# Kernel optimization log

Hardware: AMD Instinct MI355X
Metric: run time of the kernel (lower is better)

## Reference

```python
import jax, jax.numpy as jnp
import numpy as np

B, T_ENC, T_DEC = 64, 512, 400
IN_DIM, R = 80, 2
D_ENC, D_ATT, D_PRE = 256, 256, 128
NEG_INF = -1e9


def _gru(x, h, Wi, Wh, bi, bh):
    # PyTorch GRUCell math
    gi = x @ Wi + bi
    gh = h @ Wh + bh
    ir, iz, inn = jnp.split(gi, 3, axis=-1)
    hr, hz, hn = jnp.split(gh, 3, axis=-1)
    r = jax.nn.sigmoid(ir + hr)
    z = jax.nn.sigmoid(iz + hz)
    n = jnp.tanh(inn + r * hn)
    return (1.0 - z) * n + z * h


def setup_inputs() -> dict:
    key = jax.random.key(0)
    ks = jax.random.split(key, 32)
    s = 0.05
    d_in = IN_DIM * R
    inp = {
        "encoder_outputs": jax.random.normal(ks[0], (B, T_ENC, D_ENC), jnp.float32),
        "inputs": jax.random.normal(ks[1], (B, T_DEC, d_in), jnp.float32),
        "memory_lengths": jax.random.randint(ks[2], (B,), T_ENC // 2, T_ENC + 1).astype(jnp.int32),
        # prenet
        "pre_W1": s * jax.random.normal(ks[3], (d_in, 256), jnp.float32),
        "pre_b1": jnp.zeros((256,), jnp.float32),
        "pre_W2": s * jax.random.normal(ks[4], (256, 128), jnp.float32),
        "pre_b2": jnp.zeros((128,), jnp.float32),
        # Bahdanau attention
        "mem_W": s * jax.random.normal(ks[5], (D_ENC, D_ATT), jnp.float32),
        "q_W": s * jax.random.normal(ks[6], (256, D_ATT), jnp.float32),
        "v_W": s * jax.random.normal(ks[7], (D_ATT, 1), jnp.float32),
        # attention GRUCell: input = cat(prenet 128, attention 256) = 384
        "att_Wi": s * jax.random.normal(ks[8], (384, 768), jnp.float32),
        "att_Wh": s * jax.random.normal(ks[9], (256, 768), jnp.float32),
        "att_bi": jnp.zeros((768,), jnp.float32),
        "att_bh": jnp.zeros((768,), jnp.float32),
        # project_to_decoder_in
        "proj_in_W": s * jax.random.normal(ks[10], (512, 256), jnp.float32),
        "proj_in_b": jnp.zeros((256,), jnp.float32),
        # decoder GRUCells
        "dec1_Wi": s * jax.random.normal(ks[11], (256, 768), jnp.float32),
        "dec1_Wh": s * jax.random.normal(ks[12], (256, 768), jnp.float32),
        "dec1_bi": jnp.zeros((768,), jnp.float32),
        "dec1_bh": jnp.zeros((768,), jnp.float32),
        "dec2_Wi": s * jax.random.normal(ks[13], (256, 768), jnp.float32),
        "dec2_Wh": s * jax.random.normal(ks[14], (256, 768), jnp.float32),
        "dec2_bi": jnp.zeros((768,), jnp.float32),
        "dec2_bh": jnp.zeros((768,), jnp.float32),
        # output projections
        "mel_W": s * jax.random.normal(ks[15], (256, d_in), jnp.float32),
        "mel_b": jnp.zeros((d_in,), jnp.float32),
        "gate_W": s * jax.random.normal(ks[16], (256, R), jnp.float32),
        "gate_b": jnp.zeros((R,), jnp.float32),
    }
    return inp


def _decoder_forward(encoder_outputs, inputs, memory_lengths,
                     pre_W1, pre_b1, pre_W2, pre_b2,
                     mem_W, q_W, v_W,
                     att_Wi, att_Wh, att_bi, att_bh,
                     proj_in_W, proj_in_b,
                     dec1_Wi, dec1_Wh, dec1_bi, dec1_bh,
                     dec2_Wi, dec2_Wh, dec2_bi, dec2_bh,
                     mel_W, mel_b, gate_W, gate_b):
    Bq, Tq, _ = encoder_outputs.shape
    processed_memory = encoder_outputs @ mem_W  # (B, T_enc, D_att)
    valid = jnp.arange(Tq)[None, :] < memory_lengths[:, None]  # (B, T_enc)

    # teacher forcing: input at step t is inputs[t-1], zeros at t=0
    prev = jnp.concatenate([jnp.zeros_like(inputs[:, :1]), inputs[:, :-1]], axis=1)
    prev = jnp.swapaxes(prev, 0, 1)  # (T_dec, B, in_dim*r)

    def prenet(x):
        # dropout is identity in eval mode
        h = jax.nn.relu(x @ pre_W1 + pre_b1)
        return jax.nn.relu(h @ pre_W2 + pre_b2)

    def step(carry, x_prev):
        att_h, h1, h2, cur_att = carry
        pre = prenet(x_prev)  # (B, 128)
        cell_in = jnp.concatenate([pre, cur_att], axis=-1)  # (B, 384)
        att_h = _gru(cell_in, att_h, att_Wi, att_Wh, att_bi, att_bh)  # (B, 256)
        # Bahdanau alignment over encoder memory
        score = jnp.squeeze(
            jnp.tanh(processed_memory + (att_h @ q_W)[:, None, :]) @ v_W, -1)  # (B, T_enc)
        score = jnp.where(valid, score, NEG_INF)
        align = jax.nn.softmax(score, axis=-1)
        cur_att = jnp.einsum('bt,btd->bd', align, encoder_outputs)  # (B, 256)
        dec_in = jnp.concatenate([att_h, cur_att], axis=-1) @ proj_in_W + proj_in_b
        h1 = _gru(dec_in, h1, dec1_Wi, dec1_Wh, dec1_bi, dec1_bh)
        d = h1 + dec_in
        h2 = _gru(d, h2, dec2_Wi, dec2_Wh, dec2_bi, dec2_bh)
        d = h2 + d
        gate = jax.nn.sigmoid(d @ gate_W + gate_b)  # (B, r)
        out = d @ mel_W + mel_b  # (B, in_dim*r)
        return (att_h, h1, h2, cur_att), (out, align, gate)

    z = jnp.zeros((Bq, 256), encoder_outputs.dtype)
    init = (z, z, z, z)
    _, (outs, aligns, gates) = jax.lax.scan(step, init, prev)
    outputs = jnp.swapaxes(outs, 0, 1)      # (B, T_dec, in_dim*r)
    alignments = jnp.swapaxes(aligns, 0, 1)  # (B, T_dec, T_enc)
    gates = jnp.swapaxes(gates, 0, 1)        # (B, T_dec, r)
    return outputs, alignments, gates


def reference(encoder_outputs, inputs, memory_lengths,
              pre_W1, pre_b1, pre_W2, pre_b2,
              mem_W, q_W, v_W,
              att_Wi, att_Wh, att_bi, att_bh,
              proj_in_W, proj_in_b,
              dec1_Wi, dec1_Wh, dec1_bi, dec1_bh,
              dec2_Wi, dec2_Wh, dec2_bi, dec2_bh,
              mel_W, mel_b, gate_W, gate_b):
    return _decoder_forward(encoder_outputs, inputs, memory_lengths,
                            pre_W1, pre_b1, pre_W2, pre_b2,
                            mem_W, q_W, v_W,
                            att_Wi, att_Wh, att_bi, att_bh,
                            proj_in_W, proj_in_b,
                            dec1_Wi, dec1_Wh, dec1_bi, dec1_bh,
                            dec2_Wi, dec2_Wh, dec2_bi, dec2_bh,
                            mel_W, mel_b, gate_W, gate_b)
```

## Files before the change

kernel.cpp:

```cpp
#include <hip/hip_runtime.h>

#define TDEC 400
#define NTH 512
#define NWG 256

typedef float f32x4 __attribute__((ext_vector_type(4)));
typedef unsigned u32x4 __attribute__((ext_vector_type(4)));
typedef unsigned u32x2 __attribute__((ext_vector_type(2)));

#define OFF_BAR   0
#define OFF_ATTH  11264
#define OFF_H1    44032
#define OFF_H2    76800
#define OFF_CURP  109568
#define OFF_ATTS  125952
#define OFF_Q     126208
#define ZERO_FLOATS 142592
#define OFF_D1    142592
#define OFF_SUMS  158976
#define OFF_C1    184576
#define OFF_PRE   185600
#define OFF_PMB   1824000
#define OFF_ENCB  6018304
#define OFF_D2A   10212608
#define T_WIT_A   10212608
#define T_WHT_A   10507520
#define T_M1T     10704128
#define T_WHT1    11097344
#define T_PJT     11293952
#define T_WIT2    11425024
#define T_WHT2    11621632
#define T_QWT     11818240
#define T_M1      11883776
#define OFF_BLOB  16766208

#define BLOB_N   26112
#define BLOB_STR 26624
#define BO_AI  0
#define BO_AH  4608
#define BO_Q   7680
#define BO_M1  8704
#define BO_H1  14848
#define BO_PJ  17920
#define BO_I2  19968
#define BO_H2  23040

#define AOFF 4096000
#define GOFF 17203200

#define MSTI  (8*1024)
#define GENI  (9*1024)
#define FAILI (10*1024)

__device__ __forceinline__ float fsig(float x){ return 1.0f/(1.0f+__expf(-x)); }
__device__ __forceinline__ float ftanh(float x){ float e = __expf(2.0f*x); return 1.0f - 2.0f/(e+1.0f); }
__device__ __forceinline__ float blo(unsigned u){ return __uint_as_float(u<<16); }
__device__ __forceinline__ float bhi(unsigned u){ return __uint_as_float(u & 0xffff0000u); }

__device__ __forceinline__ f32x4 cload16(const float* p){
  f32x4 r;
  asm volatile("global_load_dwordx4 %0, %1, off sc0 sc1" : "=v"(r) : "v"(p));
  return r;
}
__device__ __forceinline__ f32x4 cload16w(const float* p){
  f32x4 r;
  asm volatile("global_load_dwordx4 %0, %1, off sc0 sc1\n\ts_waitcnt vmcnt(0)" : "=v"(r) : "v"(p));
  return r;
}
__device__ __forceinline__ u32x4 cload16u(const unsigned short* p){
  u32x4 r;
  asm volatile("global_load_dwordx4 %0, %1, off sc0 sc1" : "=v"(r) : "v"(p));
  return r;
}
__device__ __forceinline__ float aload4(const float* p){
  unsigned u = __hip_atomic_load((const unsigned*)p, __ATOMIC_RELAXED, __HIP_MEMORY_SCOPE_AGENT);
  return __uint_as_float(u);
}
__device__ __forceinline__ void astore4(float* p, float v){
  __hip_atomic_store((unsigned*)p, __float_as_uint(v), __ATOMIC_RELAXED, __HIP_MEMORY_SCOPE_AGENT);
}
__device__ __forceinline__ void aadd(float* p, float v){
  __hip_atomic_fetch_add(p, v, __ATOMIC_RELAXED, __HIP_MEMORY_SCOPE_AGENT);
}
__device__ __forceinline__ int aloadi(const int* p){
  return __hip_atomic_load(p, __ATOMIC_RELAXED, __HIP_MEMORY_SCOPE_AGENT);
}

__device__ __forceinline__ void ldsbar(){
  __builtin_amdgcn_sched_barrier(0);
  asm volatile("s_waitcnt lgkmcnt(0)" ::: "memory");
  __builtin_amdgcn_s_barrier();
  __builtin_amdgcn_sched_barrier(0);
}

__device__ __forceinline__ void gbar(int* bar, int wg, int n){
  asm volatile("s_waitcnt vmcnt(0)" ::: "memory");
  __syncthreads();
  if (threadIdx.x == 0){
    if (aloadi(&bar[FAILI]) == 0){
      int a = __hip_atomic_fetch_add(&bar[(wg&7)*1024], 1, __ATOMIC_RELAXED, __HIP_MEMORY_SCOPE_AGENT);
      if (a == 32*n - 1){
        int m = __hip_atomic_fetch_add(&bar[MSTI], 1, __ATOMIC_RELAXED, __HIP_MEMORY_SCOPE_AGENT);
        if (m == 8*n - 1)
          __hip_atomic_store(&bar[GENI], n, __ATOMIC_RELAXED, __HIP_MEMORY_SCOPE_AGENT);
      }
      int sp = 0;
      while (aloadi(&bar[GENI]) < n){
        __builtin_amdgcn_s_sleep(1);
        if (++sp > (1<<20)){
          __hip_atomic_store(&bar[FAILI], 1, __ATOMIC_RELAXED, __HIP_MEMORY_SCOPE_AGENT);
          break;
        }
      }
    }
  }
  __syncthreads();
}

__device__ __forceinline__ unsigned short f2bf(float f){
  unsigned u = __float_as_uint(f);
  return (unsigned short)((u + 0x7fffu + ((u>>16)&1u)) >> 16);
}

template<int N8>
__device__ __forceinline__ float bdot(const unsigned short* wr, const float* xr){
  f32x4 accA = 0.f, accB = 0.f;
  #pragma unroll 4
  for (int k = 0; k < N8; ++k){
    u32x4 u = *(const u32x4*)(wr + k*8);
    f32x4 a = *(const f32x4*)(xr + k*8);
    f32x4 b = *(const f32x4*)(xr + k*8 + 4);
    f32x4 w0, w1;
    w0[0]=blo(u[0]); w0[1]=bhi(u[0]); w0[2]=blo(u[1]); w0[3]=bhi(u[1]);
    w1[0]=blo(u[2]); w1[1]=bhi(u[2]); w1[2]=blo(u[3]); w1[3]=bhi(u[3]);
    accA += w0*a; accB += w1*b;
  }
  f32x4 s = accA + accB;
  return s[0]+s[1]+s[2]+s[3];
}

__global__ __launch_bounds__(256, 1) void transpose_k(const float* __restrict__ in,
                                                      float* __restrict__ outp, int K, int C){
  __shared__ float tl[32][33];
  int c0 = blockIdx.x * 32, k0 = blockIdx.y * 32;
  int tx = threadIdx.x & 31, ty = threadIdx.x >> 5;
  for (int i = ty; i < 32; i += 8){
    int k = k0 + i, c = c0 + tx;
    if (k < K && c < C) tl[i][tx] = in[k * C + c];
  }
  __syncthreads();
  for (int i = ty; i < 32; i += 8){
    int c = c0 + i, k = k0 + tx;
    if (c < C && k < K) outp[c * K + k] = tl[tx][i];
  }
}

__global__ __launch_bounds__(128, 1) void fuse_k(const float* __restrict__ projW,
    const float* __restrict__ d1Wi, float* __restrict__ M1){
  int jt = blockIdx.x % 6, i = blockIdx.x / 6;
  int j = jt * 128 + threadIdx.x;
  float acc = 0.f;
  for (int k = 0; k < 256; ++k) acc += projW[i*256+k] * d1Wi[k*768+j];
  M1[i*768+j] = acc;
}

__global__ __launch_bounds__(256, 1) void c1_k(const float* __restrict__ projB,
    const float* __restrict__ d1Wi, const float* __restrict__ d1Bi, float* __restrict__ C1){
  int j = blockIdx.x * 256 + threadIdx.x;
  float acc = d1Bi[j];
  for (int k = 0; k < 256; ++k) acc += projB[k] * d1Wi[k*768+j];
  C1[j] = acc;
}

__global__ __launch_bounds__(512, 1) void pack_k(float* __restrict__ ws){
  int sl = blockIdx.x;
  const float* TAI = ws + T_WIT_A;
  const float* TAH = ws + T_WHT_A;
  const float* TM1 = ws + T_M1T;
  const float* TH1 = ws + T_WHT1;
  const float* TPJ = ws + T_PJT;
  const float* TI2 = ws + T_WIT2;
  const float* TH2 = ws + T_WHT2;
  const float* TQ  = ws + T_QWT;
  unsigned short* blob = (unsigned short*)(ws + OFF_BLOB) + (size_t)sl * BLOB_STR;
  for (int idx = threadIdx.x; idx < BLOB_N; idx += 512){
    float v; int cs, k, o;
    if (idx < BO_AH){ cs = idx / 384; k = idx - cs*384;
      v = TAI[((cs%3)*256 + sl*4 + cs/3)*384 + k]; }
    else if (idx < BO_Q){ o = idx - BO_AH; cs = o >> 8; k = o & 255;
      v = TAH[((cs%3)*256 + sl*4 + cs/3)*256 + k]; }
    else if (idx < BO_M1){ o = idx - BO_Q; cs = o >> 8; k = o & 255;
      v = TQ[(sl*4 + cs)*256 + k]; }
    else if (idx < BO_H1){ o = idx - BO_M1; cs = o >> 9; k = o & 511;
      v = TM1[((cs%3)*256 + sl*4 + cs/3)*512 + k]; }
    else if (idx < BO_PJ){ o = idx - BO_H1; cs = o >> 8; k = o & 255;
      v = TH1[((cs%3)*256 + sl*4 + cs/3)*256 + k]; }
    else if (idx < BO_I2){ o = idx - BO_PJ; cs = o >> 9; k = o & 511;
      v = TPJ[(sl*4 + cs)*512 + k]; }
    else if (idx < BO_H2){ o = idx - BO_I2; cs = o >> 8; k = o & 255;
      v = TI2[((cs%3)*256 + sl*4 + cs/3)*256 + k]; }
    else { o = idx - BO_H2; cs = o >> 8; k = o & 255;
      v = TH2[((cs%3)*256 + sl*4 + cs/3)*256 + k]; }
    blob[idx] = f2bf(v);
  }
}

__global__ __launch_bounds__(256, 1) void qt_k(const float* __restrict__ ws,
                                               float* __restrict__ out){
  unsigned short* qtb = (unsigned short*)(out + GOFF);
  const float* TQ = ws + T_QWT;
  int idx = blockIdx.x * 256 + threadIdx.x;
  int it = idx >> 11, j = (idx >> 3) & 255, e = idx & 7;
  qtb[idx] = f2bf(TQ[j*256 + it*8 + e]);
}

__global__ __launch_bounds__(NTH, 1) void prenet_k(float* __restrict__ ws,
    const float* __restrict__ inp, const float* __restrict__ W1, const float* __restrict__ B1,
    const float* __restrict__ W2, const float* __restrict__ B2){
  __shared__ float xT[160 * 33];
  __shared__ float hT[256 * 33];
  int t = blockIdx.x, half = blockIdx.y, tid = threadIdx.x;
  int bbase = half * 32;
  for (int r = tid; r < 32 * 160; r += NTH){
    int b2 = r / 160; int k = r - b2 * 160;
    xT[k * 33 + b2] = (t == 0) ? 0.f : inp[((bbase + b2) * TDEC + (t - 1)) * 160 + k];
  }
  __syncthreads();
  int bl = tid & 31, slot = tid >> 5;
  float acc1[16];
  #pragma unroll
  for (int i = 0; i < 16; ++i) acc1[i] = 0.f;
  for (int k = 0; k < 160; ++k){
    float xv = xT[k * 33 + bl];
    const float* wr = W1 + k * 256 + slot * 16;
    #pragma unroll
    for (int i = 0; i < 16; ++i) acc1[i] += xv * wr[i];
  }
  #pragma unroll
  for (int i = 0; i < 16; ++i){
    int c = slot * 16 + i;
    hT[c * 33 + bl] = fmaxf(acc1[i] + B1[c], 0.f);
  }
  __syncthreads();
  float acc2[8];
  #pragma unroll
  for (int i = 0; i < 8; ++i) acc2[i] = 0.f;
  for (int k = 0; k < 256; ++k){
    float hv = hT[k * 33 + bl];
    const float* wr = W2 + k * 128 + slot * 8;
    #pragma unroll
    for (int i = 0; i < 8; ++i) acc2[i] += hv * wr[i];
  }
  unsigned short* dst = (unsigned short*)(ws + OFF_PRE) + (size_t)t*8192 + (bbase + bl)*128 + slot*8;
  u32x4 pk;
  #pragma unroll
  for (int i = 0; i < 4; ++i){
    float v0 = fmaxf(acc2[2*i] + B2[slot*8 + 2*i], 0.f);
    float v1 = fmaxf(acc2[2*i+1] + B2[slot*8 + 2*i+1], 0.f);
    pk[i] = (unsigned)f2bf(v0) | ((unsigned)f2bf(v1) << 16);
  }
  *(u32x4*)dst = pk;
}

__global__ __launch_bounds__(NTH, 1) void pm_k(float* __restrict__ ws,
    const float* __restrict__ enc, const float* __restrict__ memW){
  int wg = blockIdx.x, tid = threadIdx.x;
  int b = wg & 63, th = wg >> 6;
  int slot = tid & 7, tt = tid >> 3;
  int trow = th * 64 + tt;
  const float* er = enc + ((size_t)(b * 512 + trow)) * 256;
  f32x4 acc[8];
  #pragma unroll
  for (int i = 0; i < 8; ++i) acc[i] = 0.f;
  for (int k = 0; k < 256; ++k){
    float ev = er[k];
    const f32x4* wr = (const f32x4*)(memW + k * 256 + slot * 32);
    #pragma unroll
    for (int i = 0; i < 8; ++i) acc[i] += ev * wr[i];
  }
  unsigned short* pmB = (unsigned short*)(ws + OFF_PMB);
  unsigned short* dst = pmB + ((size_t)(b * 512 + trow)) * 256 + slot * 32;
  #pragma unroll
  for (int i = 0; i < 8; ++i){
    u32x2 pk;
    pk[0] = (unsigned)f2bf(acc[i][0]) | ((unsigned)f2bf(acc[i][1]) << 16);
    pk[1] = (unsigned)f2bf(acc[i][2]) | ((unsigned)f2bf(acc[i][3]) << 16);
    *(u32x2*)(dst + i * 4) = pk;
  }
  const float* e2 = enc + ((size_t)(b * 512 + th * 64)) * 256;
  unsigned* eb = (unsigned*)((unsigned short*)(ws + OFF_ENCB) + ((size_t)(b * 512 + th * 64)) * 256);
  for (int i = tid; i < 64 * 128; i += NTH){
    float v0 = e2[i * 2], v1 = e2[i * 2 + 1];
    eb[i] = (unsigned)f2bf(v0) | ((unsigned)f2bf(v1) << 16);
  }
}

__global__ __launch_bounds__(NTH, 2) void decoder_k(
    float* __restrict__ ws, float* __restrict__ out,
    const int* __restrict__ memlen,
    const float* __restrict__ vW,
    const float* __restrict__ attBi, const float* __restrict__ attBh,
    const float* __restrict__ projB,
    const float* __restrict__ d1Bh,
    const float* __restrict__ d2Bi, const float* __restrict__ d2Bh)
{
  const int wg = blockIdx.x, tid = threadIdx.x;
  int* bar = (int*)ws;
  float* attH = ws + OFF_ATTH;
  float* h1a  = ws + OFF_H1;
  float* h2a  = ws + OFF_H2;
  float* const curB[2]  = { ws + OFF_CURP, ws + OFF_Q };
  float* const attSB[2] = { ws + OFF_ATTS, ws + OFF_ATTS + 64 };
  float* d1v  = ws + OFF_D1;
  const float* C1v = ws + OFF_C1;
  const unsigned short* preB16 = (const unsigned short*)(ws + OFF_PRE);
  const unsigned short* pmB  = (const unsigned short*)(ws + OFF_PMB);
  const unsigned short* encB = (const unsigned short*)(ws + OFF_ENCB);
  const unsigned short* qtb = (const unsigned short*)(out + GOFF);
  float* d2a  = ws + OFF_D2A;

  __shared__ float BUF[12416];
  __shared__ float qL[256], vL[256];
  __shared__ float eL[128];
  __shared__ float ewGi[192], ewGh[192], pdec[128];

  if (tid < 256) vL[tid] = vW[tid];

  const int bg = wg & 3, sl = wg >> 2;
  const int b0 = bg << 4;
  const int b2 = wg & 63, ch2 = wg >> 6;
  const int len2 = memlen[b2];
  const unsigned short* blob = (const unsigned short*)(ws + OFF_BLOB) + (size_t)sl * BLOB_STR;

  const int bq = tid & 15, x = tid >> 4;
  const int cs = (x >= 12) ? (x - 12) : x;
  const int gg = cs % 3, jh = cs / 3;
  const int col = gg * 256 + sl * 4 + jh;

  const int r0 = tid >> 6, c0 = (tid & 63) << 2;
  const int r1 = r0 + 8;
  const int prr = tid >> 4, pcc = (tid & 15) * 8;

  u32x4 pmv[8], env[8];
  {
    int te = tid >> 2, part = tid & 3;
    const u32x4* pmp = (const u32x4*)(pmB + ((size_t)(b2*512 + ch2*128 + te))*256 + part*64);
    #pragma unroll
    for (int i = 0; i < 8; ++i) pmv[i] = pmp[i];
    int ich = tid >> 5, dblk = tid & 31;
    const unsigned short* ep = encB + ((size_t)(b2*512 + ch2*128 + ich*8))*256 + dblk*8;
    #pragma unroll
    for (int i = 0; i < 8; ++i) env[i] = *(const u32x4*)(ep + i*256);
  }

  f32x4 pH0, pH1, pC0, pC1;
  float pS0, pS1;
  u32x4 ppre = 0u;
  {
    const float* gHn = attH + 16384 + b0*256;
    const float* gCn = curB[1] + b0*256;
    pH0 = cload16(gHn + (r0<<8) + c0); pH1 = cload16(gHn + (r1<<8) + c0);
    pC0 = cload16(gCn + (r0<<8) + c0); pC1 = cload16(gCn + (r1<<8) + c0);
    pS0 = aload4(attSB[1] + b0 + r0);  pS1 = aload4(attSB[1] + b0 + r1);
    if (tid < 256) ppre = cload16u(preB16 + (b0 + prr)*128 + pcc);
  }

  int bn = 0;
  for (int t = 0; t < TDEC; ++t){
    const int w = t & 1, rb = w ^ 1;

    {
      float* xL = BUF;
      float* hL = BUF + 6208;
      asm volatile("s_waitcnt vmcnt(0)" : "+v"(pH0),"+v"(pH1),"+v"(pC0),"+v"(pC1),"+v"(ppre));
      float iv0 = pS0 > 0.f ? 1.f/pS0 : 0.f, iv1 = pS1 > 0.f ? 1.f/pS1 : 0.f;
      if (tid < 256){
        float* xd = xL + prr*388 + pcc;
        xd[0]=blo(ppre[0]); xd[1]=bhi(ppre[0]); xd[2]=blo(ppre[1]); xd[3]=bhi(ppre[1]);
        xd[4]=blo(ppre[2]); xd[5]=bhi(ppre[2]); xd[6]=blo(ppre[3]); xd[7]=bhi(ppre[3]);
      }
      *(f32x4*)(hL + r0*260 + c0) = pH0; *(f32x4*)(hL + r1*260 + c0) = pH1;
      *(f32x4*)(xL + r0*388 + 128 + c0) = pC0*iv0; *(f32x4*)(xL + r1*388 + 128 + c0) = pC1*iv1;
      if (tid < 64) astore4(curB[w] + wg*64 + tid, 0.f);
      if (sl == 0 && tid < 16) astore4(attSB[w] + b0 + tid, 0.f);
      ldsbar();
      if (x < 12)
        ewGi[cs*16 + bq] = bdot<48>(blob + BO_AI + cs*384, xL + bq*388) + attBi[col];
      else if (x < 24)
        ewGh[cs*16 + bq] = bdot<32>(blob + BO_AH + cs*256, hL + bq*260) + attBh[col];
      ldsbar();
      if (tid < 64){
        int bt = tid & 15, jj = tid >> 4;
        int j = sl*4 + jj;
        float ir = ewGi[(jj*3+0)*16+bt] + ewGh[(jj*3+0)*16+bt];
        float iz = ewGi[(jj*3+1)*16+bt] + ewGh[(jj*3+1)*16+bt];
        float inn = ewGi[(jj*3+2)*16+bt];
        float hn  = ewGh[(jj*3+2)*16+bt];
        float rg = fsig(ir), z = fsig(iz);
        float n = ftanh(inn + rg * hn);
        float h = hL[bt*260 + j];
        astore4(attH + w*16384 + (b0+bt)*256 + j, (1.f - z)*n + z*h);
      }
    }
    gbar(bar, wg, ++bn);

    {
      float* ctxP = BUF;
      float* qIn  = BUF + 8192;
      if (tid < 64){
        f32x4 v = cload16w(attH + w*16384 + b2*256 + tid*4);
        *(f32x4*)(qIn + tid*4) = v;
      }
      ldsbar();
      if (tid < 256){
        const unsigned short* qw = qtb + tid*8;
        f32x4 aA = 0.f, aB = 0.f;
        #pragma unroll 4
        for (int it = 0; it < 32; ++it){
          u32x4 u = *(const u32x4*)(qw + (size_t)it*2048);
          f32x4 a = *(const f32x4*)(qIn + it*8);
          f32x4 b = *(const f32x4*)(qIn + it*8 + 4);
          f32x4 w0, w1;
          w0[0]=blo(u[0]); w0[1]=bhi(u[0]); w0[2]=blo(u[1]); w0[3]=bhi(u[1]);
          w1[0]=blo(u[2]); w1[1]=bhi(u[2]); w1[2]=blo(u[3]); w1[3]=bhi(u[3]);
          aA += w0*a; aB += w1*b;
        }
        f32x4 s4 = aA + aB;
        qL[tid] = s4[0]+s4[1]+s4[2]+s4[3];
      }
      ldsbar();
      {
        int te = tid >> 2, part = tid & 3;
        int ge = ch2*128 + te;
        float a4 = 0.f;
        #pragma unroll
        for (int i = 0; i < 8; ++i){
          u32x4 u = pmv[i];
          int kb = part*64 + i*8;
          a4 += ftanh(blo(u[0]) + qL[kb+0]) * vL[kb+0];
          a4 += ftanh(bhi(u[0]) + qL[kb+1]) * vL[kb+1];
          a4 += ftanh(blo(u[1]) + qL[kb+2]) * vL[kb+2];
          a4 += ftanh(bhi(u[1]) + qL[kb+3]) * vL[kb+3];
          a4 += ftanh(blo(u[2]) + qL[kb+4]) * vL[kb+4];
          a4 += ftanh(bhi(u[2]) + qL[kb+5]) * vL[kb+5];
          a4 += ftanh(blo(u[3]) + qL[kb+6]) * vL[kb+6];
          a4 += ftanh(bhi(u[3]) + qL[kb+7]) * vL[kb+7];
        }
        a4 += __shfl_xor(a4, 1);
        a4 += __shfl_xor(a4, 2);
        float e = (ge < len2) ? __expf(a4) : 0.f;
        if (part == 0){
          eL[te] = e;
          out[AOFF + ((size_t)(b2*TDEC + t))*512 + ge] = e;
        }
      }
      ldsbar();
      if (tid < 64){
        float s = eL[tid] + eL[tid + 64];
        #pragma unroll
        for (int o = 32; o > 0; o >>= 1) s += __shfl_down(s, o);
        if (tid == 0) aadd(attSB[w] + b2, s);
      }
      {
        int ich = tid >> 5, dblk = tid & 31;
        f32x4 acA = 0.f, acB = 0.f;
        #pragma unroll
        for (int i = 0; i < 8; ++i){
          u32x4 u = env[i];
          float e = eL[ich*8 + i];
          acA[0] += e*blo(u[0]); acA[1] += e*bhi(u[0]);
          acA[2] += e*blo(u[1]); acA[3] += e*bhi(u[1]);
          acB[0] += e*blo(u[2]); acB[1] += e*bhi(u[2]);
          acB[2] += e*blo(u[3]); acB[3] += e*bhi(u[3]);
        }
        *(f32x4*)(ctxP + tid*8) = acA;
        *(f32x4*)(ctxP + tid*8 + 4) = acB;
      }
      ldsbar();
      if (tid < 256){
        int dblk = tid >> 3, d = tid & 7;
        float s = 0.f;
        #pragma unroll
        for (int i = 0; i < 16; ++i) s += ctxP[i*256 + dblk*8 + d];
        aadd(curB[w] + b2*256 + dblk*8 + d, s);
      }
    }
    gbar(bar, wg, ++bn);

    {
      float* yL  = BUF;
      float* h1L = BUF + 8256;
      const float* gA = attH + w*16384 + b0*256;
      const float* gH = h1a + rb*16384 + b0*256;
      const float* gC = curB[w] + b0*256;
      f32x4 vA0 = cload16(gA + (r0<<8) + c0), vA1 = cload16(gA + (r1<<8) + c0);
      f32x4 vH0 = cload16(gH + (r0<<8) + c0), vH1 = cload16(gH + (r1<<8) + c0);
      f32x4 vC0 = cload16(gC + (r0<<8) + c0), vC1 = cload16(gC + (r1<<8) + c0);
      float s0 = aload4(attSB[w] + b0 + r0), s1 = aload4(attSB[w] + b0 + r1);
      asm volatile("s_waitcnt vmcnt(0)" : "+v"(vA0),"+v"(vA1),"+v"(vH0),"+v"(vH1),"+v"(vC0),"+v"(vC1));
      float iv0 = s0 > 0.f ? 1.f/s0 : 0.f, iv1 = s1 > 0.f ? 1.f/s1 : 0.f;
      *(f32x4*)(yL + r0*516 + c0) = vA0;       *(f32x4*)(yL + r1*516 + c0) = vA1;
      *(f32x4*)(h1L + r0*260 + c0) = vH0;      *(f32x4*)(h1L + r1*260 + c0) = vH1;
      *(f32x4*)(yL + r0*516 + 256 + c0) = vC0*iv0; *(f32x4*)(yL + r1*516 + 256 + c0) = vC1*iv1;
      ldsbar();
      if (x < 12)
        ewGi[cs*16 + bq] = bdot<64>(blob + BO_M1 + cs*512, yL + bq*516) + C1v[col];
      else if (x < 24)
        ewGh[cs*16 + bq] = bdot<32>(blob + BO_H1 + cs*256, h1L + bq*260) + d1Bh[col];
      else {
        int idx = tid - 384;
        int bq2 = idx & 15, cc = (idx >> 4) & 3, half = idx >> 6;
        pdec[idx] = bdot<32>(blob + BO_PJ + cc*512 + half*256, yL + bq2*516 + half*256);
      }
      ldsbar();
      if (tid < 64){
        int bt = tid & 15, jj = tid >> 4;
        int j = sl*4 + jj;
        float ir = ewGi[(jj*3+0)*16+bt] + ewGh[(jj*3+0)*16+bt];
        float iz = ewGi[(jj*3+1)*16+bt] + ewGh[(jj*3+1)*16+bt];
        float inn = ewGi[(jj*3+2)*16+bt];
        float hn  = ewGh[(jj*3+2)*16+bt];
        float rg = fsig(ir), z = fsig(iz);
        float n = ftanh(inn + rg * hn);
        float hv = h1L[bt*260 + j];
        float hnew = (1.f - z)*n + z*hv;
        float dec = pdec[jj*16 + bt] + pdec[64 + jj*16 + bt] + projB[j];
        astore4(h1a + w*16384 + (b0+bt)*256 + j, hnew);
        astore4(d1v + (b0+bt)*256 + j, hnew + dec);
      }
      if (sl == 0 && tid < 16)
        ws[OFF_SUMS + t*64 + b0 + tid] = aload4(attSB[w] + b0 + tid);
    }
    gbar(bar, wg, ++bn);

    {
      float* dL  = BUF;
      float* h2L = BUF + 4160;
      const float* gD = d1v + b0*256;
      const float* gH = h2a + rb*16384 + b0*256;
      f32x4 vD0 = cload16(gD + (r0<<8) + c0), vD1 = cload16(gD + (r1<<8) + c0);
      f32x4 vH0 = cload16(gH + (r0<<8) + c0), vH1 = cload16(gH + (r1<<8) + c0);
      asm volatile("s_waitcnt vmcnt(0)" : "+v"(vD0),"+v"(vD1),"+v"(vH0),"+v"(vH1));
      {
        const float* gHn = attH + w*16384 + b0*256;
        const float* gCn = curB[w] + b0*256;
        pH0 = cload16(gHn + (r0<<8) + c0); pH1 = cload16(gHn + (r1<<8) + c0);
        pC0 = cload16(gCn + (r0<<8) + c0); pC1 = cload16(gCn + (r1<<8) + c0);
        pS0 = aload4(attSB[w] + b0 + r0);  pS1 = aload4(attSB[w] + b0 + r1);
        int tn = (t + 1 < TDEC) ? (t + 1) : 0;
        if (tid < 256) ppre = cload16u(preB16 + (size_t)tn*8192 + (b0 + prr)*128 + pcc);
      }
      *(f32x4*)(dL + r0*260 + c0) = vD0;  *(f32x4*)(dL + r1*260 + c0) = vD1;
      *(f32x4*)(h2L + r0*260 + c0) = vH0; *(f32x4*)(h2L + r1*260 + c0) = vH1;
      ldsbar();
      if (x < 12)
        ewGi[cs*16 + bq] = bdot<32>(blob + BO_I2 + cs*256, dL + bq*260) + d2Bi[col];
      else if (x < 24)
        ewGh[cs*16 + bq] = bdot<32>(blob + BO_H2 + cs*256, h2L + bq*260) + d2Bh[col];
      ldsbar();
      if (tid < 64){
        int bt = tid & 15, jj = tid >> 4;
        int j = sl*4 + jj;
        float ir = ewGi[(jj*3+0)*16+bt] + ewGh[(jj*3+0)*16+bt];
        float iz = ewGi[(jj*3+1)*16+bt] + ewGh[(jj*3+1)*16+bt];
        float inn = ewGi[(jj*3+2)*16+bt];
        float hn  = ewGh[(jj*3+2)*16+bt];
        float rg = fsig(ir), z = fsig(iz);
        float n = ftanh(inn + rg * hn);
        float hv = h2L[bt*260 + j];
        float hnew = (1.f - z)*n + z*hv;
        astore4(h2a + w*16384 + (b0+bt)*256 + j, hnew);
        d2a[t*16384 + j*64 + (b0+bt)] = hnew + dL[bt*260 + j];
      }
      ldsbar();
    }
  }
}

__global__ __launch_bounds__(NTH, 1) void rescale_k(const float* __restrict__ ws,
                                                    float* __restrict__ out){
  int blk = blockIdx.x;
  int b = blk / TDEC, t = blk - b * TDEC;
  float s = ws[OFF_SUMS + t*64 + b];
  float inv = (s > 0.f) ? 1.f/s : 0.f;
  out[AOFF + (size_t)blk*512 + threadIdx.x] *= inv;
}

__global__ __launch_bounds__(NTH, 1) void outproj_k(const float* __restrict__ ws,
    float* __restrict__ out, const float* __restrict__ melW, const float* __restrict__ melB,
    const float* __restrict__ gateW, const float* __restrict__ gateB){
  int t = blockIdx.x, tid = threadIdx.x;
  int cx = tid & 255, bh = tid >> 8;
  const float* src = ws + OFF_D2A + t*16384 + bh*32;
  float acc[32];
  #pragma unroll
  for (int i = 0; i < 32; ++i) acc[i] = 0.f;
  bool ismel = (cx < 160);
  bool isgate = (cx >= 160 && cx < 162);
  for (int j = 0; j < 256; ++j){
    float wv = 0.f;
    if (ismel) wv = melW[j*160 + cx];
    else if (isgate) wv = gateW[j*2 + (cx - 160)];
    const f32x4* dp = (const f32x4*)(src + j*64);
    f32x4 vv[8];
    #pragma unroll
    for (int q = 0; q < 8; ++q) vv[q] = dp[q];
    #pragma unroll
    for (int q = 0; q < 8; ++q){
      acc[q*4+0] += vv[q][0]*wv; acc[q*4+1] += vv[q][1]*wv;
      acc[q*4+2] += vv[q][2]*wv; acc[q*4+3] += vv[q][3]*wv;
    }
  }
  if (ismel){
    float bb = melB[cx];
    #pragma unroll
    for (int i = 0; i < 32; ++i){
      int b = bh*32 + i;
      out[((size_t)(b*TDEC + t))*160 + cx] = acc[i] + bb;
    }
  } else if (isgate){
    int g = cx - 160;
    float bb = gateB[g];
    #pragma unroll
    for (int i = 0; i < 32; ++i){
      int b = bh*32 + i;
      out[GOFF + ((size_t)(b*TDEC + t))*2 + g] = fsig(acc[i] + bb);
    }
  }
}

extern "C" void kernel_launch(void* const* d_in, const int* in_sizes, int n_in,
                              void* d_out, int out_size, void* d_ws, size_t ws_size,
                              hipStream_t stream)
{
  (void)in_sizes; (void)n_in; (void)out_size; (void)ws_size;
  const float* enc   = (const float*)d_in[0];
  const float* inp   = (const float*)d_in[1];
  const int*   mlen  = (const int*)d_in[2];
  const float* preW1 = (const float*)d_in[3];
  const float* preB1 = (const float*)d_in[4];
  const float* preW2 = (const float*)d_in[5];
  const float* preB2 = (const float*)d_in[6];
  const float* memW  = (const float*)d_in[7];
  const float* qW    = (const float*)d_in[8];
  const float* vW    = (const float*)d_in[9];
  const float* attWi = (const float*)d_in[10];
  const float* attWh = (const float*)d_in[11];
  const float* attBi = (const float*)d_in[12];
  const float* attBh = (const float*)d_in[13];
  const float* projW = (const float*)d_in[14];
  const float* projB = (const float*)d_in[15];
  const float* d1Wi  = (const float*)d_in[16];
  const float* d1Wh  = (const float*)d_in[17];
  const float* d1Bi  = (const float*)d_in[18];
  const float* d1Bh  = (const float*)d_in[19];
  const float* d2Wi  = (const float*)d_in[20];
  const float* d2Wh  = (const float*)d_in[21];
  const float* d2Bi  = (const float*)d_in[22];
  const float* d2Bh  = (const float*)d_in[23];
  const float* melW  = (const float*)d_in[24];
  const float* melB  = (const float*)d_in[25];
  const float* gateW = (const float*)d_in[26];
  const float* gateB = (const float*)d_in[27];
  float* ws = (float*)d_ws;
  float* out = (float*)d_out;

  hipMemsetAsync(d_ws, 0, (size_t)ZERO_FLOATS * sizeof(float), stream);

  dim3 tt(256);
  transpose_k<<<dim3(24, 12), tt, 0, stream>>>(attWi, ws + T_WIT_A, 384, 768);
  transpose_k<<<dim3(24, 8),  tt, 0, stream>>>(attWh, ws + T_WHT_A, 256, 768);
  transpose_k<<<dim3(24, 8),  tt, 0, stream>>>(d1Wh,  ws + T_WHT1, 256, 768);
  transpose_k<<<dim3(24, 8),  tt, 0, stream>>>(d2Wi,  ws + T_WIT2, 256, 768);
  transpose_k<<<dim3(24, 8),  tt, 0, stream>>>(d2Wh,  ws + T_WHT2, 256, 768);
  transpose_k<<<dim3(8, 16),  tt, 0, stream>>>(projW, ws + T_PJT, 512, 256);
  transpose_k<<<dim3(8, 8),   tt, 0, stream>>>(qW,    ws + T_QWT, 256, 256);
  fuse_k<<<3072, 128, 0, stream>>>(projW, d1Wi, ws + T_M1);
  c1_k<<<3, 256, 0, stream>>>(projB, d1Wi, d1Bi, ws + OFF_C1);
  transpose_k<<<dim3(24, 16), tt, 0, stream>>>(ws + T_M1, ws + T_M1T, 512, 768);
  pack_k<<<64, NTH, 0, stream>>>(ws);
  qt_k<<<256, 256, 0, stream>>>(ws, out);

  prenet_k<<<dim3(TDEC, 2), NTH, 0, stream>>>(ws, inp, preW1, preB1, preW2, preB2);
  pm_k<<<512, NTH, 0, stream>>>(ws, enc, memW);
  decoder_k<<<NWG, NTH, 0, stream>>>(ws, out, mlen, vW, attBi, attBh, projB,
                                     d1Bh, d2Bi, d2Bh);
  rescale_k<<<64 * TDEC, NTH, 0, stream>>>(ws, out);
  outproj_k<<<TDEC, NTH, 0, stream>>>(ws, out, melW, melB, gateW, gateB);
}
```

Baseline: 14.44 ms.

## Partition grid barrier into independent batch groups and split query projection

Workgroups are remapped so that each group of 64 workgroups handles one 16-batch slice end to end, including its attention rows. The global barrier is replaced by a per-group barrier with its own counters and generation flag, so each synchronization waits on 64 workgroups instead of 256. The query projection now uses all 512 threads, each doing half the reduction, and combines the halves through a new LDS buffer. This costs one extra LDS barrier per step and depends on there being no data dependencies across batch groups.

```diff
diff --git a/kernel.cpp b/kernel.cpp
--- a/kernel.cpp
+++ b/kernel.cpp
@@ -93,19 +93,19 @@
   __builtin_amdgcn_sched_barrier(0);
 }
 
-__device__ __forceinline__ void gbar(int* bar, int wg, int n){
+__device__ __forceinline__ void gbar(int* bar, int g, int l, int n){
   asm volatile("s_waitcnt vmcnt(0)" ::: "memory");
   __syncthreads();
   if (threadIdx.x == 0){
     if (aloadi(&bar[FAILI]) == 0){
-      int a = __hip_atomic_fetch_add(&bar[(wg&7)*1024], 1, __ATOMIC_RELAXED, __HIP_MEMORY_SCOPE_AGENT);
-      if (a == 32*n - 1){
-        int m = __hip_atomic_fetch_add(&bar[MSTI], 1, __ATOMIC_RELAXED, __HIP_MEMORY_SCOPE_AGENT);
+      int a = __hip_atomic_fetch_add(&bar[(l&7)*1024 + g*64], 1, __ATOMIC_RELAXED, __HIP_MEMORY_SCOPE_AGENT);
+      if (a == 8*n - 1){
+        int m = __hip_atomic_fetch_add(&bar[MSTI + g*64], 1, __ATOMIC_RELAXED, __HIP_MEMORY_SCOPE_AGENT);
         if (m == 8*n - 1)
-          __hip_atomic_store(&bar[GENI], n, __ATOMIC_RELAXED, __HIP_MEMORY_SCOPE_AGENT);
+          __hip_atomic_store(&bar[GENI + g*64], n, __ATOMIC_RELAXED, __HIP_MEMORY_SCOPE_AGENT);
       }
       int sp = 0;
-      while (aloadi(&bar[GENI]) < n){
+      while (aloadi(&bar[GENI + g*64]) < n){
         __builtin_amdgcn_s_sleep(1);
         if (++sp > (1<<20)){
           __hip_atomic_store(&bar[FAILI], 1, __ATOMIC_RELAXED, __HIP_MEMORY_SCOPE_AGENT);
@@ -322,13 +322,15 @@
   __shared__ float BUF[12416];
   __shared__ float qL[256], vL[256];
   __shared__ float eL[128];
+  __shared__ float red[512];
   __shared__ float ewGi[192], ewGh[192], pdec[128];
 
   if (tid < 256) vL[tid] = vW[tid];
 
-  const int bg = wg & 3, sl = wg >> 2;
-  const int b0 = bg << 4;
-  const int b2 = wg & 63, ch2 = wg >> 6;
+  const int g = wg >> 6, l = wg & 63;
+  const int sl = l;
+  const int b0 = g << 4;
+  const int b2 = b0 + (l >> 2), ch2 = l & 3;
   const int len2 = memlen[b2];
   const unsigned short* blob = (const unsigned short*)(ws + OFF_BLOB) + (size_t)sl * BLOB_STR;
 
@@ -402,7 +404,7 @@
         astore4(attH + w*16384 + (b0+bt)*256 + j, (1.f - z)*n + z*h);
       }
     }
-    gbar(bar, wg, ++bn);
+    gbar(bar, g, l, ++bn);
 
     {
       float* ctxP = BUF;
@@ -412,22 +414,26 @@
         *(f32x4*)(qIn + tid*4) = v;
       }
       ldsbar();
-      if (tid < 256){
-        const unsigned short* qw = qtb + tid*8;
+      {
+        int j = tid & 255, hf = tid >> 8;
+        const unsigned short* qw = qtb + j*8 + (size_t)hf*16*2048;
+        const float* qx = qIn + hf*128;
         f32x4 aA = 0.f, aB = 0.f;
         #pragma unroll 4
-        for (int it = 0; it < 32; ++it){
+        for (int it = 0; it < 16; ++it){
           u32x4 u = *(const u32x4*)(qw + (size_t)it*2048);
-          f32x4 a = *(const f32x4*)(qIn + it*8);
-          f32x4 b = *(const f32x4*)(qIn + it*8 + 4);
+          f32x4 a = *(const f32x4*)(qx + it*8);
+          f32x4 b = *(const f32x4*)(qx + it*8 + 4);
           f32x4 w0, w1;
           w0[0]=blo(u[0]); w0[1]=bhi(u[0]); w0[2]=blo(u[1]); w0[3]=bhi(u[1]);
           w1[0]=blo(u[2]); w1[1]=bhi(u[2]); w1[2]=blo(u[3]); w1[3]=bhi(u[3]);
           aA += w0*a; aB += w1*b;
         }
         f32x4 s4 = aA + aB;
-        qL[tid] = s4[0]+s4[1]+s4[2]+s4[3];
-      }
+        red[tid] = s4[0]+s4[1]+s4[2]+s4[3];
+      }
+      ldsbar();
+      if (tid < 256) qL[tid] = red[tid] + red[tid + 256];
       ldsbar();
       {
         int te = tid >> 2, part = tid & 3;
@@ -485,7 +491,7 @@
         aadd(curB[w] + b2*256 + dblk*8 + d, s);
       }
     }
-    gbar(bar, wg, ++bn);
+    gbar(bar, g, l, ++bn);
 
     {
       float* yL  = BUF;
@@ -531,7 +537,7 @@
       if (sl == 0 && tid < 16)
         ws[OFF_SUMS + t*64 + b0 + tid] = aload4(attSB[w] + b0 + tid);
     }
-    gbar(bar, wg, ++bn);
+    gbar(bar, g, l, ++bn);
 
     {
       float* dL  = BUF;
```

New measurement: 13.32 ms. -7.7%, faster.
